# Performance work log

Hardware: AMD Instinct MI355X
Metric: run time of the kernel (lower is better)

Reference implementation:

```python
import jax, jax.numpy as jnp
import numpy as np

N = 50000        # nodes
E = 800000       # edges (before self loops)
G = 512          # graphs
H = 2            # heads
FIN = 128        # in_features
CH = 64          # hidden per head
COUT = 32        # out_features
NEG_SLOPE = 0.2  # PyG GATConv default
BN_EPS = 1e-5


def _gat(x, src, dst, W, a_src, a_dst, b, concat, n):
    # x: [n, F], W: [F, H*C], a_src/a_dst: [H, C]
    h = (x @ W).reshape(n, a_src.shape[0], a_src.shape[1])        # [n, H, C]
    e = jax.nn.leaky_relu((h * a_src).sum(-1)[src]
                          + (h * a_dst).sum(-1)[dst], NEG_SLOPE)  # [Etot, H]
    # per-destination segment softmax (self loops guarantee nonempty segments)
    m = jax.ops.segment_max(e, dst, num_segments=n)
    ex = jnp.exp(e - m[dst])
    s = jax.ops.segment_sum(ex, dst, num_segments=n)
    alpha = ex / (s[dst] + 1e-16)                                 # [Etot, H]
    out = jax.ops.segment_sum(h[src] * alpha[:, :, None], dst, num_segments=n)
    out = out.reshape(n, -1) if concat else out.mean(axis=1)
    return out + b


def _bn(x, gamma, beta, mean, var):
    # BatchNorm1d in eval mode (running statistics)
    return (x - mean) * jax.lax.rsqrt(var + BN_EPS) * gamma + beta


def setup_inputs() -> dict:
    key = jax.random.key(0)
    ks = jax.random.split(key, 12)
    x = jax.random.normal(ks[0], (N, FIN), dtype=jnp.float32)
    edge_index = jax.random.randint(ks[1], (2, E), 0, N, dtype=jnp.int32)
    batch = jnp.sort(jax.random.randint(ks[2], (N,), 0, G, dtype=jnp.int32))
    inp = {"x": x, "edge_index": edge_index, "batch": batch}
    # layer 1: GATConv(FIN -> CH, heads=H, concat=True)
    inp["W1"] = jax.random.normal(ks[3], (FIN, H * CH), dtype=jnp.float32) * 0.1
    inp["as1"] = jax.random.normal(ks[4], (H, CH), dtype=jnp.float32) * 0.1
    inp["ad1"] = jax.random.normal(ks[5], (H, CH), dtype=jnp.float32) * 0.1
    inp["b1"] = jnp.zeros((H * CH,), dtype=jnp.float32)
    inp["bn1_gamma"] = jnp.ones((H * CH,), dtype=jnp.float32)
    inp["bn1_beta"] = jnp.zeros((H * CH,), dtype=jnp.float32)
    inp["bn1_mean"] = jax.random.normal(ks[6], (H * CH,), dtype=jnp.float32) * 0.05
    inp["bn1_var"] = jnp.ones((H * CH,), dtype=jnp.float32)
    # layer 2: GATConv(H*CH -> COUT, heads=H, concat=False)
    inp["W2"] = jax.random.normal(ks[7], (H * CH, H * COUT), dtype=jnp.float32) * 0.1
    inp["as2"] = jax.random.normal(ks[8], (H, COUT), dtype=jnp.float32) * 0.1
    inp["ad2"] = jax.random.normal(ks[9], (H, COUT), dtype=jnp.float32) * 0.1
    inp["b2"] = jnp.zeros((COUT,), dtype=jnp.float32)
    inp["bn2_gamma"] = jnp.ones((COUT,), dtype=jnp.float32)
    inp["bn2_beta"] = jnp.zeros((COUT,), dtype=jnp.float32)
    inp["bn2_mean"] = jax.random.normal(ks[10], (COUT,), dtype=jnp.float32) * 0.05
    inp["bn2_var"] = jnp.ones((COUT,), dtype=jnp.float32)
    return inp


def reference(x, edge_index, batch,
              W1, as1, ad1, b1, bn1_gamma, bn1_beta, bn1_mean, bn1_var,
              W2, as2, ad2, b2, bn2_gamma, bn2_beta, bn2_mean, bn2_var):
    n = x.shape[0]
    sl = jnp.arange(n, dtype=edge_index.dtype)
    src = jnp.concatenate([edge_index[0], sl])  # PyG add_self_loops=True
    dst = jnp.concatenate([edge_index[1], sl])
    h = _gat(x, src, dst, W1, as1, ad1, b1, True, n)
    h = jax.nn.relu(_bn(h, bn1_gamma, bn1_beta, bn1_mean, bn1_var))
    h = _gat(h, src, dst, W2, as2, ad2, b2, False, n)
    h = _bn(h, bn2_gamma, bn2_beta, bn2_mean, bn2_var)
    # global mean pool over graphs
    sums = jax.ops.segment_sum(h, batch, num_segments=G)
    cnts = jax.ops.segment_sum(jnp.ones((n,), h.dtype), batch, num_segments=G)
    pooled = sums / jnp.maximum(cnts, 1.0)[:, None]
    return jax.nn.log_softmax(pooled, axis=1)
```

## Files before the change

### kernel.cpp

```cpp
#include <hip/hip_runtime.h>
#include <hip/hip_bf16.h>

#define NEG_SLOPE 0.2f
#define BN_EPS 1e-5f
#define BSHIFT 7
#define P_PART 256
#define MAXB 512

typedef unsigned int uint32;
typedef unsigned short ushort16;
typedef __attribute__((ext_vector_type(8))) short bf16x8;
typedef __attribute__((ext_vector_type(4))) float f32x4;
typedef __attribute__((ext_vector_type(2))) float f32x2;

__device__ __forceinline__ ushort16 f2bf(float f) {
    uint32 u = __float_as_uint(f);
    u = (u + 0x7fff + ((u >> 16) & 1)) >> 16;
    return (ushort16)u;
}

__device__ __forceinline__ f32x2 pkfma(f32x2 ex2, uint32 u, f32x2 acc) {
    f32x2 f;
    f.x = __uint_as_float(u << 16);
    f.y = __uint_as_float(u & 0xffff0000u);
    asm("v_pk_fma_f32 %0, %1, %2, %0" : "+v"(acc) : "v"(ex2), "v"(f));
    return acc;
}

__device__ __forceinline__ void scan_bbase(const int* __restrict__ rowtot, int nbuck,
                                           int Etot, int* sb ) {
    const int t = threadIdx.x;
    int v0 = (t < nbuck) ? rowtot[t] : 0;
    int v1 = (256 + t < nbuck) ? rowtot[256 + t] : 0;
    sb[t] = v0;
    sb[256 + t] = v1;
    __syncthreads();
    for (int off = 1; off < 512; off <<= 1) {
        int a0 = (t >= off) ? sb[t - off] : 0;
        int a1 = (256 + t >= off) ? sb[256 + t - off] : 0;
        __syncthreads();
        sb[t] += a0;
        sb[256 + t] += a1;
        __syncthreads();
    }
    int i0 = sb[t], i1 = sb[256 + t];
    __syncthreads();
    sb[t] = i0 - v0;
    sb[256 + t] = i1 - v1;
    if (t == 0) sb[MAXB] = Etot;
    __syncthreads();
}

template <int OC, int C>
__device__ __forceinline__ void pack_col(int col, int k, const float* __restrict__ W,
                                         const float* __restrict__ a_s,
                                         const float* __restrict__ a_d,
                                         ushort16* __restrict__ wt) {
    float v = 0.f;
    if (col < OC) {
        v = W[k * OC + col];
    } else if (col < OC + 2) {
        int hh = col - OC;
        float s = 0.f;
        for (int c = 0; c < C; ++c) s += W[k * OC + hh * C + c] * a_s[hh * C + c];
        v = s;
    } else if (col < OC + 4) {
        int hh = col - OC - 2;
        float s = 0.f;
        for (int c = 0; c < C; ++c) s += W[k * OC + hh * C + c] * a_d[hh * C + c];
        v = s;
    }
    wt[(size_t)col * 128 + k] = f2bf(v);
}

template <int OC, int NT, bool AF32>
__device__ __forceinline__ void gemm_body(int gb, const void* __restrict__ xin,
                                          const ushort16* __restrict__ wt,
                                          ushort16* __restrict__ h, float4* __restrict__ att,
                                          float2* __restrict__ asc, int N) {
    const int wave = threadIdx.x >> 6, lane = threadIdx.x & 63;
    const int tile = gb * 4 + wave;
    if (tile * 16 >= N) return;
    const int m = lane & 15, quad = lane >> 4;
    const int node = tile * 16 + m;

    bf16x8 a[4];
    if (AF32) {
        const float* xr = (const float*)xin + (size_t)node * 128 + quad * 8;
#pragma unroll
        for (int c = 0; c < 4; ++c) {
            float4 u = *(const float4*)(xr + c * 32);
            float4 v = *(const float4*)(xr + c * 32 + 4);
            bf16x8 t;
            t[0] = (short)f2bf(u.x); t[1] = (short)f2bf(u.y);
            t[2] = (short)f2bf(u.z); t[3] = (short)f2bf(u.w);
            t[4] = (short)f2bf(v.x); t[5] = (short)f2bf(v.y);
            t[6] = (short)f2bf(v.z); t[7] = (short)f2bf(v.w);
            a[c] = t;
        }
    } else {
        const ushort16* xr = (const ushort16*)xin + (size_t)node * 128 + quad * 8;
#pragma unroll
        for (int c = 0; c < 4; ++c) a[c] = *(const bf16x8*)(xr + c * 32);
    }

    for (int t = 0; t < NT; ++t) {
        const ushort16* wr = wt + ((size_t)(t * 16 + m)) * 128 + quad * 8;
        bf16x8 b[4];
#pragma unroll
        for (int c = 0; c < 4; ++c) b[c] = *(const bf16x8*)(wr + c * 32);
        f32x4 acc = {0.f, 0.f, 0.f, 0.f};
#pragma unroll
        for (int c = 0; c < 4; ++c)
            acc = __builtin_amdgcn_mfma_f32_16x16x32_bf16(a[c], b[c], acc, 0, 0, 0);
        if (t * 16 < OC) {
#pragma unroll
            for (int r = 0; r < 4; ++r) {
                int nrow = tile * 16 + quad * 4 + r;
                h[(size_t)nrow * OC + t * 16 + m] = f2bf(acc[r]);
            }
        } else if (m < 4) {
#pragma unroll
            for (int r = 0; r < 4; ++r) {
                int nrow = tile * 16 + quad * 4 + r;
                ((float*)(att + nrow))[m] = acc[r];
                if (m < 2) ((float*)(asc + nrow))[m] = acc[r];
            }
        }
    }
}

__global__ __launch_bounds__(256) void fused_prep(
    const int* __restrict__ ei, int E, int Etot, int nbuck, int chunk, int* __restrict__ hist,
    const float* __restrict__ W1, const float* __restrict__ as1, const float* __restrict__ ad1,
    ushort16* __restrict__ wt1,
    const float* __restrict__ W2, const float* __restrict__ as2, const float* __restrict__ ad2,
    ushort16* __restrict__ wt2,
    const float* __restrict__ b1, const float* __restrict__ g1, const float* __restrict__ be1,
    const float* __restrict__ mu1, const float* __restrict__ vr1,
    const float* __restrict__ b2, const float* __restrict__ g2, const float* __restrict__ be2,
    const float* __restrict__ mu2, const float* __restrict__ vr2,
    float2* __restrict__ bn1, float2* __restrict__ bn2,
    const int* __restrict__ batch, int N, int G, int* __restrict__ gstart) {
    const int bid = blockIdx.x;
    if (bid < P_PART) {
        __shared__ int lh[MAXB];
        const int p = bid;
        for (int i = threadIdx.x; i < nbuck; i += 256) lh[i] = 0;
        __syncthreads();
        const int beg = p * chunk;
        const int end = min(beg + chunk, Etot);
        for (int i = beg + threadIdx.x; i < end; i += 256) {
            int d = (i < E) ? ei[E + i] : i - E;
            atomicAdd(&lh[d >> BSHIFT], 1);
        }
        __syncthreads();
        for (int i = threadIdx.x; i < nbuck; i += 256) hist[(size_t)i * P_PART + p] = lh[i];
        return;
    }
    int rb = bid - P_PART;
    if (rb < 72) {
        pack_col<128, 64>(rb * 2 + (threadIdx.x >> 7), threadIdx.x & 127, W1, as1, ad1, wt1);
        return;
    }
    rb -= 72;
    if (rb < 40) {
        pack_col<64, 32>(rb * 2 + (threadIdx.x >> 7), threadIdx.x & 127, W2, as2, ad2, wt2);
        return;
    }
    rb -= 40;
    if (rb == 0) {
        const int c = threadIdx.x;
        if (c < 128) {
            float A = g1[c] * rsqrtf(vr1[c] + BN_EPS);
            bn1[c] = make_float2(A, A * (b1[c] - mu1[c]) + be1[c]);
        } else if (c < 160) {
            const int c2 = c - 128;
            float A = g2[c2] * rsqrtf(vr2[c2] + BN_EPS);
            bn2[c2] = make_float2(A, A * (b2[c2] - mu2[c2]) + be2[c2]);
        }
        return;
    }
    rb -= 1;
    {
        int g = rb * 256 + (int)threadIdx.x;
        if (g > G) return;
        if (g == G) { gstart[G] = N; return; }
        int lo = 0, hi = N;
        while (lo < hi) { int mid = (lo + hi) >> 1; if (batch[mid] < g) lo = mid + 1; else hi = mid; }
        gstart[g] = lo;
    }
}

__global__ __launch_bounds__(P_PART) void row_scan(int* __restrict__ hist,
                                                   int* __restrict__ rowtot) {
    const int b = blockIdx.x;
    __shared__ int s[P_PART];
    const int t = threadIdx.x;
    int v = hist[(size_t)b * P_PART + t];
    s[t] = v;
    __syncthreads();
    for (int off = 1; off < P_PART; off <<= 1) {
        int u = (t >= off) ? s[t - off] : 0;
        __syncthreads();
        s[t] += u;
        __syncthreads();
    }
    hist[(size_t)b * P_PART + t] = s[t] - v;
    if (t == P_PART - 1) rowtot[b] = s[t];
}

__global__ __launch_bounds__(256) void fused_scatter_gemm1(
    const int* __restrict__ ei, int E, int Etot, int nbuck, int chunk,
    const int* __restrict__ hist, const int* __restrict__ rowtot, uint32* __restrict__ ebuf,
    const void* __restrict__ x, const ushort16* __restrict__ wt1,
    ushort16* __restrict__ h1, float4* __restrict__ att1, float2* __restrict__ asc1, int N) {
    const int bid = blockIdx.x;
    if (bid < P_PART) {
        __shared__ int sb[MAXB + 1];
        __shared__ int cur[MAXB];
        scan_bbase(rowtot, nbuck, Etot, sb);
        const int p = bid;
        for (int i = threadIdx.x; i < nbuck; i += 256)
            cur[i] = sb[i] + hist[(size_t)i * P_PART + p];
        __syncthreads();
        const int beg = p * chunk;
        const int end = min(beg + chunk, Etot);
        for (int i = beg + threadIdx.x; i < end; i += 256) {
            int s_, d_;
            if (i < E) { s_ = ei[i]; d_ = ei[E + i]; }
            else       { s_ = d_ = i - E; }
            int pos = atomicAdd(&cur[d_ >> BSHIFT], 1);
            ebuf[pos] = ((uint32)(d_ & ((1 << BSHIFT) - 1)) << 25) | (uint32)s_;
        }
    } else {
        gemm_body<128, 9, true>(bid - P_PART, x, wt1, h1, att1, asc1, N);
    }
}

__global__ __launch_bounds__(256) void bucket_place(
    const int* __restrict__ rowtot, int nbuck, int Etot, const uint32* __restrict__ ebuf,
    int N, int* __restrict__ base, int* __restrict__ csr_src) {
    const int bk = blockIdx.x;
    __shared__ int sb[MAXB + 1];
    __shared__ int ldeg[1 << BSHIFT];
    __shared__ int sscan[1 << BSHIFT];
    __shared__ int lcur[1 << BSHIFT];
    scan_bbase(rowtot, nbuck, Etot, sb);
    const int t = threadIdx.x;
    if (t < (1 << BSHIFT)) { ldeg[t] = 0; lcur[t] = 0; }
    __syncthreads();
    const int beg = sb[bk], end = sb[bk + 1];
    for (int i = beg + t; i < end; i += 256) atomicAdd(&ldeg[ebuf[i] >> 25], 1);
    __syncthreads();
    if (t < 128) sscan[t] = ldeg[t];
    __syncthreads();
    for (int off = 1; off < 128; off <<= 1) {
        int v = 0;
        if (t < 128 && t >= off) v = sscan[t - off];
        __syncthreads();
        if (t < 128) sscan[t] += v;
        __syncthreads();
    }
    if (t < 128) {
        int node = (bk << BSHIFT) + t;
        if (node < N) base[node] = beg + sscan[t] - ldeg[t];
    }
    __syncthreads();
    for (int i = beg + t; i < end; i += 256) {
        uint32 pk = ebuf[i];
        int dl = (int)(pk >> 25);
        int s_ = (int)(pk & 0x1FFFFFFu);
        int pos = beg + (sscan[dl] - ldeg[dl]) + atomicAdd(&lcur[dl], 1);
        csr_src[pos] = s_;
    }
}

__global__ __launch_bounds__(256) void gemm2_kernel(
    const void* __restrict__ xin, const ushort16* __restrict__ wt,
    ushort16* __restrict__ h, float4* __restrict__ att, float2* __restrict__ asc, int N) {
    gemm_body<64, 5, false>(blockIdx.x, xin, wt, h, att, asc, N);
}

__global__ __launch_bounds__(256) void gat_gather1(
    const int* __restrict__ base, const int* __restrict__ csr_src, int Etot, int N,
    const ushort16* __restrict__ h, const float4* __restrict__ att,
    const float2* __restrict__ asc, const float2* __restrict__ bn1,
    ushort16* __restrict__ outb) {
    const int tid = threadIdx.x;
    const int node = blockIdx.x * 16 + (tid >> 4);
    if (node >= N) return;
    const int t = tid & 63;
    const int q = tid & 15;
    const int gbase = t & 48;
    const int hh = q >> 3;
    const int hbit = q & 8;
    const int eh = q & 7;
    const int beg = base[node];
    const int end = (node + 1 < N) ? base[node + 1] : Etot;
    const int deg = end - beg;
    const float4 adn = att[node];
    const float ad = hh ? adn.w : adn.z;
    const char* hq = (const char*)h + q * 16;

    f32x2 ac0 = {0.f, 0.f}, ac1 = {0.f, 0.f}, ac2 = {0.f, 0.f}, ac3 = {0.f, 0.f};
    float ssum = 0.f;

    for (int c0e = 0; c0e < deg; c0e += 8) {
        const int degc = min(deg - c0e, 8);
        const bool ok = eh < degc;
        const int sidxme = csr_src[beg + c0e + (ok ? eh : 0)];
        const int offme = sidxme << 8;
        float e = ((const float*)asc)[2 * sidxme + hh] + ad;
        e = e > 0.f ? e : NEG_SLOPE * e;
        const float x = ok ? __expf(e) : 0.f;
        float r = x;
#pragma unroll
        for (int off = 1; off < 8; off <<= 1) r += __shfl_xor(r, off, 64);
        ssum += r;
        for (int e0 = 0; e0 < degc; e0 += 4) {
            int offv[4];
            float exv[4];
            uint4 hv[4];
#pragma unroll
            for (int j = 0; j < 4; ++j) {
                const int s = e0 + j;
                offv[j] = __shfl(offme, gbase + s, 64);
                exv[j] = __shfl(x, (gbase + s) | hbit, 64);
                hv[j] = *(const uint4*)(hq + offv[j]);
            }
#pragma unroll
            for (int j = 0; j < 4; ++j) {
                f32x2 ex2; ex2.x = exv[j]; ex2.y = exv[j];
                ac0 = pkfma(ex2, hv[j].x, ac0);
                ac1 = pkfma(ex2, hv[j].y, ac1);
                ac2 = pkfma(ex2, hv[j].z, ac2);
                ac3 = pkfma(ex2, hv[j].w, ac3);
            }
        }
    }
    const float inv = 1.f / (ssum + 1e-16f);
    const int c0 = 8 * q;
    const float4* bp = (const float4*)(bn1 + c0);
    const float4 w0 = bp[0], w1 = bp[1], w2 = bp[2], w3 = bp[3];
    float va[8] = {ac0.x, ac0.y, ac1.x, ac1.y, ac2.x, ac2.y, ac3.x, ac3.y};
    float Ac[8] = {w0.x, w0.z, w1.x, w1.z, w2.x, w2.z, w3.x, w3.z};
    float Cc[8] = {w0.y, w0.w, w1.y, w1.w, w2.y, w2.w, w3.y, w3.w};
    uint32 pk[4];
#pragma unroll
    for (int i = 0; i < 8; i += 2) {
        float v0 = fmaxf(fmaf(Ac[i], va[i] * inv, Cc[i]), 0.f);
        float v1 = fmaxf(fmaf(Ac[i + 1], va[i + 1] * inv, Cc[i + 1]), 0.f);
        pk[i >> 1] = (uint32)f2bf(v0) | ((uint32)f2bf(v1) << 16);
    }
    *(uint4*)(outb + (size_t)node * 128 + c0) = make_uint4(pk[0], pk[1], pk[2], pk[3]);
}

__global__ __launch_bounds__(256) void gat_gather2(
    const int* __restrict__ base, const int* __restrict__ csr_src, int Etot, int N,
    const ushort16* __restrict__ h2, const float4* __restrict__ att,
    const float2* __restrict__ asc, const float2* __restrict__ bn2,
    float* __restrict__ node_out) {
    const int tid = threadIdx.x;
    const int node = blockIdx.x * 16 + (tid >> 4);
    if (node >= N) return;
    const int t = tid & 63;
    const int q = tid & 15;
    const int gbase = t & 48;
    const int hh = q >> 3;
    const int hbit = q & 8;
    const int eh = q & 7;
    const int beg = base[node];
    const int end = (node + 1 < N) ? base[node + 1] : Etot;
    const int deg = end - beg;
    const float4 adn = att[node];
    const float ad = hh ? adn.w : adn.z;
    const char* hq = (const char*)h2 + q * 8;

    f32x2 ac0 = {0.f, 0.f}, ac1 = {0.f, 0.f};
    float ssum = 0.f;

    for (int c0e = 0; c0e < deg; c0e += 8) {
        const int degc = min(deg - c0e, 8);
        const bool ok = eh < degc;
        const int sidxme = csr_src[beg + c0e + (ok ? eh : 0)];
        const int offme = sidxme << 7;
        float e = ((const float*)asc)[2 * sidxme + hh] + ad;
        e = e > 0.f ? e : NEG_SLOPE * e;
        const float x = ok ? __expf(e) : 0.f;
        float r = x;
#pragma unroll
        for (int off = 1; off < 8; off <<= 1) r += __shfl_xor(r, off, 64);
        ssum += r;
        for (int e0 = 0; e0 < degc; e0 += 4) {
            int offv[4];
            float exv[4];
            uint2 hv[4];
#pragma unroll
            for (int j = 0; j < 4; ++j) {
                const int s = e0 + j;
                offv[j] = __shfl(offme, gbase + s, 64);
                exv[j] = __shfl(x, (gbase + s) | hbit, 64);
                hv[j] = *(const uint2*)(hq + offv[j]);
            }
#pragma unroll
            for (int j = 0; j < 4; ++j) {
                f32x2 ex2; ex2.x = exv[j]; ex2.y = exv[j];
                ac0 = pkfma(ex2, hv[j].x, ac0);
                ac1 = pkfma(ex2, hv[j].y, ac1);
            }
        }
    }
    const float inv = 1.f / (ssum + 1e-16f);
    float v0 = ac0.x * inv, v1 = ac0.y * inv, v2 = ac1.x * inv, v3 = ac1.y * inv;
    const int psrc = gbase | ((q + 8) & 15);
    float p0 = __shfl(v0, psrc, 64);
    float p1 = __shfl(v1, psrc, 64);
    float p2 = __shfl(v2, psrc, 64);
    float p3 = __shfl(v3, psrc, 64);
    if (q < 8) {
        const int c0 = 4 * q;
        const float4* bp = (const float4*)(bn2 + c0);
        const float4 w0 = bp[0], w1 = bp[1];
        float m0 = fmaf(w0.x, 0.5f * (v0 + p0), w0.y);
        float m1 = fmaf(w0.z, 0.5f * (v1 + p1), w0.w);
        float m2 = fmaf(w1.x, 0.5f * (v2 + p2), w1.y);
        float m3 = fmaf(w1.z, 0.5f * (v3 + p3), w1.w);
        *(float4*)(node_out + (size_t)node * 32 + c0) = make_float4(m0, m1, m2, m3);
    }
}

__global__ __launch_bounds__(256) void pool_logsoftmax(
    const float* __restrict__ node_out, const int* __restrict__ gstart,
    float* __restrict__ out) {
    const int gidx = blockIdx.x;
    const int tid = threadIdx.x;
    const int c = tid & 31, r = tid >> 5;
    const int n0 = gstart[gidx], n1 = gstart[gidx + 1];
    float s = 0.f;
    for (int n = n0 + r; n < n1; n += 8) s += node_out[(size_t)n * 32 + c];
    __shared__ float red[8][32];
    red[r][c] = s;
    __syncthreads();
    if (r == 0) {
        float tot = red[0][c];
#pragma unroll
        for (int k = 1; k < 8; ++k) tot += red[k][c];
        float v = tot / fmaxf((float)(n1 - n0), 1.f);
        float m = v;
#pragma unroll
        for (int off = 16; off >= 1; off >>= 1) m = fmaxf(m, __shfl_xor(m, off, 64));
        float ex = __expf(v - m);
        float ssum = ex;
#pragma unroll
        for (int off = 16; off >= 1; off >>= 1) ssum += __shfl_xor(ssum, off, 64);
        out[gidx * 32 + c] = v - m - logf(ssum);
    }
}

extern "C" void kernel_launch(void* const* d_in, const int* in_sizes, int n_in,
                              void* d_out, int out_size, void* d_ws, size_t ws_size,
                              hipStream_t stream) {
    const float* x   = (const float*)d_in[0];
    const int* ei    = (const int*)d_in[1];
    const int* batch = (const int*)d_in[2];
    const float* W1  = (const float*)d_in[3];
    const float* as1 = (const float*)d_in[4];
    const float* ad1 = (const float*)d_in[5];
    const float* b1  = (const float*)d_in[6];
    const float* g1  = (const float*)d_in[7];
    const float* be1 = (const float*)d_in[8];
    const float* mu1 = (const float*)d_in[9];
    const float* vr1 = (const float*)d_in[10];
    const float* W2  = (const float*)d_in[11];
    const float* as2 = (const float*)d_in[12];
    const float* ad2 = (const float*)d_in[13];
    const float* b2  = (const float*)d_in[14];
    const float* g2  = (const float*)d_in[15];
    const float* be2 = (const float*)d_in[16];
    const float* mu2 = (const float*)d_in[17];
    const float* vr2 = (const float*)d_in[18];
    float* out = (float*)d_out;

    const int N = in_sizes[0] / 128;
    const int E = in_sizes[1] / 2;
    const int Etot = E + N;
    const int G = out_size / 32;
    const int nbuck = (N + (1 << BSHIFT) - 1) >> BSHIFT;
    const int chunk = (Etot + P_PART - 1) / P_PART;
    const int M = nbuck * P_PART;
    const int ntile = (N + 15) / 16;
    const int gemm_grid = (ntile + 3) / 4;
    const int gbb = (G + 1 + 255) / 256;

    float* p = (float*)d_ws;
    size_t o = 0;
    auto al = [&]() { o = (o + 3) & ~(size_t)3; };
    ushort16* h1b   = (ushort16*)(p + o); o += (size_t)N * 64;  al();
    ushort16* agg1b = (ushort16*)(p + o); o += (size_t)N * 64;  al();
    ushort16* h2b   = (ushort16*)(p + o); o += (size_t)N * 32;  al();
    float4* att1 = (float4*)(p + o); o += (size_t)N * 4;  al();
    float4* att2 = (float4*)(p + o); o += (size_t)N * 4;  al();
    float2* asc1 = (float2*)(p + o); o += (size_t)N * 2;  al();
    float2* asc2 = (float2*)(p + o); o += (size_t)N * 2;  al();
    float* nodeo = p + o; o += (size_t)N * 32; al();
    ushort16* wt1 = (ushort16*)(p + o); o += (size_t)144 * 64; al();
    ushort16* wt2 = (ushort16*)(p + o); o += (size_t)80 * 64;  al();
    float2* bn1  = (float2*)(p + o); o += (size_t)128 * 2; al();
    float2* bn2  = (float2*)(p + o); o += (size_t)32 * 2;  al();
    int* csr_src = (int*)(p + o); o += (size_t)Etot; al();
    uint32* ebuf = (uint32*)(p + o); o += (size_t)Etot; al();
    int* base    = (int*)(p + o); o += (size_t)N;    al();
    int* hist    = (int*)(p + o); o += (size_t)M;    al();
    int* rowtot  = (int*)(p + o); o += (size_t)nbuck + 4; al();
    int* gstart  = (int*)(p + o); o += (size_t)G + 4; al();

    fused_prep<<<P_PART + 72 + 40 + 1 + gbb, 256, 0, stream>>>(
        ei, E, Etot, nbuck, chunk, hist, W1, as1, ad1, wt1, W2, as2, ad2, wt2,
        b1, g1, be1, mu1, vr1, b2, g2, be2, mu2, vr2, bn1, bn2,
        batch, N, G, gstart);
    row_scan<<<nbuck, P_PART, 0, stream>>>(hist, rowtot);
    fused_scatter_gemm1<<<P_PART + gemm_grid, 256, 0, stream>>>(
        ei, E, Etot, nbuck, chunk, hist, rowtot, ebuf, x, wt1, h1b, att1, asc1, N);
    bucket_place<<<nbuck, 256, 0, stream>>>(rowtot, nbuck, Etot, ebuf, N, base, csr_src);
    gat_gather1<<<(N + 15) / 16, 256, 0, stream>>>(base, csr_src, Etot, N, h1b, att1, asc1,
                                                   bn1, agg1b);
    gemm2_kernel<<<gemm_grid, 256, 0, stream>>>(agg1b, wt2, h2b, att2, asc2, N);
    gat_gather2<<<(N + 15) / 16, 256, 0, stream>>>(base, csr_src, Etot, N, h2b, att2, asc2,
                                                   bn2, nodeo);
    pool_logsoftmax<<<G, 256, 0, stream>>>(nodeo, gstart, out);
}
```

Measured before the change: 218.6 us.

## Prefetch next edge chunk indices and batch all eight row gathers per chunk

In both GAT aggregation kernels, the CSR source index for the next 8-edge chunk is now loaded one iteration early, so the dependent gather does not wait on an index load. All eight neighbour feature rows per chunk are issued together before the exp and reduction work, instead of in groups of four after it. This is meant to raise memory-level parallelism and hide the latency of the irregular gathers. In exchange it uses more registers (eight vector loads held at once), which may lower occupancy, and it issues loads for padding lanes in partial chunks.

Result: faster. 211.9 us (-3.1%).

```diff
diff --git a/kernel.cpp b/kernel.cpp
--- a/kernel.cpp
+++ b/kernel.cpp
@@ -306,38 +306,44 @@
     f32x2 ac0 = {0.f, 0.f}, ac1 = {0.f, 0.f}, ac2 = {0.f, 0.f}, ac3 = {0.f, 0.f};
     float ssum = 0.f;
 
+    int sidxme = csr_src[beg + ((eh < deg) ? eh : 0)];
+
     for (int c0e = 0; c0e < deg; c0e += 8) {
         const int degc = min(deg - c0e, 8);
         const bool ok = eh < degc;
-        const int sidxme = csr_src[beg + c0e + (ok ? eh : 0)];
         const int offme = sidxme << 8;
-        float e = ((const float*)asc)[2 * sidxme + hh] + ad;
+        const float av = ((const float*)asc)[2 * sidxme + hh];
+        uint4 hv[8];
+#pragma unroll
+        for (int s = 0; s < 8; ++s) {
+            const int ofs = __shfl(offme, gbase + s, 64);
+            hv[s] = *(const uint4*)(hq + ofs);
+        }
+        const int nb = c0e + 8;
+        const int na = (nb < deg) ? (nb + ((eh < deg - nb) ? eh : 0)) : 0;
+        const int sidx_next = csr_src[beg + na];
+        float e = av + ad;
         e = e > 0.f ? e : NEG_SLOPE * e;
         const float x = ok ? __expf(e) : 0.f;
         float r = x;
 #pragma unroll
         for (int off = 1; off < 8; off <<= 1) r += __shfl_xor(r, off, 64);
         ssum += r;
-        for (int e0 = 0; e0 < degc; e0 += 4) {
-            int offv[4];
-            float exv[4];
-            uint4 hv[4];
-#pragma unroll
-            for (int j = 0; j < 4; ++j) {
-                const int s = e0 + j;
-                offv[j] = __shfl(offme, gbase + s, 64);
-                exv[j] = __shfl(x, (gbase + s) | hbit, 64);
-                hv[j] = *(const uint4*)(hq + offv[j]);
+#pragma unroll
+        for (int e0 = 0; e0 < 8; e0 += 4) {
+            if (e0 < degc) {
+#pragma unroll
+                for (int j = 0; j < 4; ++j) {
+                    const float ex = __shfl(x, (gbase + e0 + j) | hbit, 64);
+                    f32x2 ex2; ex2.x = ex; ex2.y = ex;
+                    ac0 = pkfma(ex2, hv[e0 + j].x, ac0);
+                    ac1 = pkfma(ex2, hv[e0 + j].y, ac1);
+                    ac2 = pkfma(ex2, hv[e0 + j].z, ac2);
+                    ac3 = pkfma(ex2, hv[e0 + j].w, ac3);
+                }
             }
-#pragma unroll
-            for (int j = 0; j < 4; ++j) {
-                f32x2 ex2; ex2.x = exv[j]; ex2.y = exv[j];
-                ac0 = pkfma(ex2, hv[j].x, ac0);
-                ac1 = pkfma(ex2, hv[j].y, ac1);
-                ac2 = pkfma(ex2, hv[j].z, ac2);
-                ac3 = pkfma(ex2, hv[j].w, ac3);
-            }
-        }
+        }
+        sidxme = sidx_next;
     }
     const float inv = 1.f / (ssum + 1e-16f);
     const int c0 = 8 * q;
@@ -380,36 +386,42 @@
     f32x2 ac0 = {0.f, 0.f}, ac1 = {0.f, 0.f};
     float ssum = 0.f;
 
+    int sidxme = csr_src[beg + ((eh < deg) ? eh : 0)];
+
     for (int c0e = 0; c0e < deg; c0e += 8) {
         const int degc = min(deg - c0e, 8);
         const bool ok = eh < degc;
-        const int sidxme = csr_src[beg + c0e + (ok ? eh : 0)];
         const int offme = sidxme << 7;
-        float e = ((const float*)asc)[2 * sidxme + hh] + ad;
+        const float av = ((const float*)asc)[2 * sidxme + hh];
+        uint2 hv[8];
+#pragma unroll
+        for (int s = 0; s < 8; ++s) {
+            const int ofs = __shfl(offme, gbase + s, 64);
+            hv[s] = *(const uint2*)(hq + ofs);
+        }
+        const int nb = c0e + 8;
+        const int na = (nb < deg) ? (nb + ((eh < deg - nb) ? eh : 0)) : 0;
+        const int sidx_next = csr_src[beg + na];
+        float e = av + ad;
         e = e > 0.f ? e : NEG_SLOPE * e;
         const float x = ok ? __expf(e) : 0.f;
         float r = x;
 #pragma unroll
         for (int off = 1; off < 8; off <<= 1) r += __shfl_xor(r, off, 64);
         ssum += r;
-        for (int e0 = 0; e0 < degc; e0 += 4) {
-            int offv[4];
-            float exv[4];
-            uint2 hv[4];
-#pragma unroll
-            for (int j = 0; j < 4; ++j) {
-                const int s = e0 + j;
-                offv[j] = __shfl(offme, gbase + s, 64);
-                exv[j] = __shfl(x, (gbase + s) | hbit, 64);
-                hv[j] = *(const uint2*)(hq + offv[j]);
+#pragma unroll
+        for (int e0 = 0; e0 < 8; e0 += 4) {
+            if (e0 < degc) {
+#pragma unroll
+                for (int j = 0; j < 4; ++j) {
+                    const float ex = __shfl(x, (gbase + e0 + j) | hbit, 64);
+                    f32x2 ex2; ex2.x = ex; ex2.y = ex;
+                    ac0 = pkfma(ex2, hv[e0 + j].x, ac0);
+                    ac1 = pkfma(ex2, hv[e0 + j].y, ac1);
+                }
             }
-#pragma unroll
-            for (int j = 0; j < 4; ++j) {
-                f32x2 ex2; ex2.x = exv[j]; ex2.y = exv[j];
-                ac0 = pkfma(ex2, hv[j].x, ac0);
-                ac1 = pkfma(ex2, hv[j].y, ac1);
-            }
-        }
+        }
+        sidxme = sidx_next;
     }
     const float inv = 1.f / (ssum + 1e-16f);
     float v0 = ac0.x * inv, v1 = ac0.y * inv, v2 = ac1.x * inv, v3 = ac1.y * inv;
```
